# Optimization experiments

Hardware: AMD Instinct MI355X
Metric: run time of the kernel (lower is better)

The kernel has to match this reference:

```python
import jax, jax.numpy as jnp
import numpy as np

B, T, D_MODEL, HEAD = 4, 4096, 1024, 64

def setup_inputs() -> dict:
    key = jax.random.key(0)
    ks = jax.random.split(key, 7)
    s = 0.02  # typical init scale
    return {
        "x":  jax.random.normal(ks[0], (B, T, D_MODEL), dtype=jnp.float32),
        "Wq": jax.random.normal(ks[1], (D_MODEL, HEAD), dtype=jnp.float32) * s,
        "bq": jnp.zeros((HEAD,), dtype=jnp.float32),
        "Wk": jax.random.normal(ks[2], (D_MODEL, HEAD), dtype=jnp.float32) * s,
        "bk": jnp.zeros((HEAD,), dtype=jnp.float32),
        "Wv": jax.random.normal(ks[3], (D_MODEL, HEAD), dtype=jnp.float32) * s,
        "bv": jnp.zeros((HEAD,), dtype=jnp.float32),
    }

def reference(x, Wq, bq, Wk, bk, Wv, bv):
    Bz, Tz, C = x.shape
    q = x @ Wq + bq                      # (B,T,H)
    k = x @ Wk + bk                      # (B,T,H)
    v = x @ Wv + bv                      # (B,T,H)
    # NOTE: original scales by sqrt(C) = sqrt(d_model), not sqrt(head_size)
    att = jnp.einsum("bth,bsh->bts", q, k) / jnp.sqrt(jnp.float32(C))
    causal = jnp.tril(jnp.ones((Tz, Tz), dtype=bool))
    att = jnp.where(causal, att, -jnp.inf)
    att = jax.nn.softmax(att, axis=-1)
    return jnp.einsum("bts,bsh->bth", att, v)  # (B,T,H)
```

## Files before the change

### kernel.cpp

```cpp
#include <hip/hip_runtime.h>
#include <hip/hip_bf16.h>
#include <hip/hip_fp16.h>

#define T_SEQ 4096
#define DMODEL 1024
#define HEAD 64
#define NBATCH 4
#define NSEG 544
#define S2LOG 0.04508422f

typedef __attribute__((ext_vector_type(8))) short bf16x8;
typedef __attribute__((ext_vector_type(4))) float f32x4;

__device__ __forceinline__ unsigned short f2bf(float f) {
    unsigned int b = __float_as_uint(f);
    unsigned int r = b + 0x7FFFu + ((b >> 16) & 1u);
    return (unsigned short)(r >> 16);
}
__device__ __forceinline__ unsigned int pk_bf16(float a, float b) {
    __hip_bfloat162 h = __float22bfloat162_rn(make_float2(a, b));
    unsigned int u; __builtin_memcpy(&u, &h, 4); return u;
}
__device__ __forceinline__ void dma16(const void* g, void* s) {
    __builtin_amdgcn_global_load_lds(
        (const __attribute__((address_space(1))) unsigned int*)g,
        (__attribute__((address_space(3))) unsigned int*)s, 16, 0, 0);
}

__global__ __launch_bounds__(256) void prep_w(
    const float* __restrict__ Wq, const float* __restrict__ Wk,
    const float* __restrict__ Wv, unsigned short* __restrict__ Wtb)
{
    __shared__ unsigned short tl[64 * 72];
    const int bid = blockIdx.x;
    const int m   = bid >> 4;
    const int k0  = (bid & 15) * 64;
    const float* W = (m == 0) ? Wq : (m == 1) ? Wk : Wv;
    const int t  = threadIdx.x;
    const int kr = t >> 2, qtr = t & 3;
#pragma unroll
    for (int i = 0; i < 4; ++i) {
        float4 wv4 = *(const float4*)&W[(k0 + kr) * 64 + qtr * 16 + i * 4];
        tl[(qtr * 16 + i * 4 + 0) * 72 + kr] = f2bf(wv4.x);
        tl[(qtr * 16 + i * 4 + 1) * 72 + kr] = f2bf(wv4.y);
        tl[(qtr * 16 + i * 4 + 2) * 72 + kr] = f2bf(wv4.z);
        tl[(qtr * 16 + i * 4 + 3) * 72 + kr] = f2bf(wv4.w);
    }
    __syncthreads();
#pragma unroll
    for (int c = 0; c < 2; ++c) {
        const int lin = c * 256 + t;
        const int n = lin >> 3, k8 = lin & 7;
        *(uint4*)&Wtb[((long)(m * 64 + n)) * 1024 + k0 + k8 * 8] =
            *(const uint4*)&tl[n * 72 + k8 * 8];
    }
}

__global__ __launch_bounds__(256, 3) void qkv_mfma(
    const float* __restrict__ x, const unsigned short* __restrict__ Wtb,
    const float* __restrict__ bq, const float* __restrict__ bk,
    const float* __restrict__ bv,
    unsigned short* __restrict__ qo, unsigned short* __restrict__ ko,
    unsigned short* __restrict__ vt)
{
    __shared__ __align__(16) float xs[2][4096];
    const int t    = threadIdx.x;
    const int lane = t & 63;
    const int l15  = lane & 15, quad = lane >> 4;
    const int w    = __builtin_amdgcn_readfirstlane(t >> 6);
    const long row0 = (long)blockIdx.x * 32;

    float bias[3];
#pragma unroll
    for (int ntl = 0; ntl < 3; ++ntl) {
        const int c = w * 48 + ntl * 16 + l15;
        bias[ntl] = (c < 64) ? bq[c] : (c < 128) ? bk[c - 64] : bv[c - 128];
    }
    f32x4 acc[2][3];
#pragma unroll
    for (int mt = 0; mt < 2; ++mt)
#pragma unroll
        for (int ntl = 0; ntl < 3; ++ntl)
            acc[mt][ntl] = (f32x4){bias[ntl], bias[ntl], bias[ntl], bias[ntl]};

    auto dma_stage = [&](int sg, int buf) {
#pragma unroll
        for (int i = 0; i < 4; ++i) {
            const int jj  = w * 4 + i;
            const int row = jj * 2 + (lane >> 5);
            const int lgb = (lane & 31) ^ (row & 7);
            dma16(x + (row0 + row) * DMODEL + sg * 128 + lgb * 4,
                  &xs[buf][jj * 256]);
        }
    };
    dma_stage(0, 0);

    for (int sg = 0; sg < 8; ++sg) {
        __syncthreads();
        if (sg + 1 < 8) dma_stage(sg + 1, (sg + 1) & 1);
        bf16x8 wf[3][4];
#pragma unroll
        for (int ntl = 0; ntl < 3; ++ntl)
#pragma unroll
            for (int kq = 0; kq < 4; ++kq)
                wf[ntl][kq] = *(const bf16x8*)&Wtb[((long)(w * 48 + ntl * 16 + l15)) * 1024
                                                   + sg * 128 + kq * 32 + quad * 8];
#pragma unroll
        for (int mt = 0; mt < 2; ++mt)
#pragma unroll
            for (int kq = 0; kq < 4; ++kq) {
                const int row  = mt * 16 + l15;
                const int b0   = (kq * 8 + quad * 2)     ^ (row & 7);
                const int b1   = (kq * 8 + quad * 2 + 1) ^ (row & 7);
                float4 a0 = *(const float4*)&xs[sg & 1][row * 128 + b0 * 4];
                float4 a1 = *(const float4*)&xs[sg & 1][row * 128 + b1 * 4];
                unsigned int u[4];
                u[0] = pk_bf16(a0.x, a0.y); u[1] = pk_bf16(a0.z, a0.w);
                u[2] = pk_bf16(a1.x, a1.y); u[3] = pk_bf16(a1.z, a1.w);
                bf16x8 a; __builtin_memcpy(&a, u, 16);
#pragma unroll
                for (int ntl = 0; ntl < 3; ++ntl)
                    acc[mt][ntl] = __builtin_amdgcn_mfma_f32_16x16x32_bf16(a, wf[ntl][kq], acc[mt][ntl], 0, 0, 0);
            }
    }
#pragma unroll
    for (int mt = 0; mt < 2; ++mt)
#pragma unroll
        for (int ntl = 0; ntl < 3; ++ntl) {
            const int c = w * 48 + ntl * 16 + l15;
            const long tr0 = row0 + mt * 16 + quad * 4;
            if (c < 64) {
#pragma unroll
                for (int r = 0; r < 4; ++r)
                    qo[(tr0 + r) * HEAD + c] = f2bf(acc[mt][ntl][r] * S2LOG);
            } else if (c < 128) {
#pragma unroll
                for (int r = 0; r < 4; ++r)
                    ko[(tr0 + r) * HEAD + (c - 64)] = f2bf(acc[mt][ntl][r]);
            } else {
                const int b = (int)(tr0 >> 12), tloc = (int)(tr0 & 4095);
                uint2 pv;
                pv.x = pk_bf16(acc[mt][ntl][0], acc[mt][ntl][1]);
                pv.y = pk_bf16(acc[mt][ntl][2], acc[mt][ntl][3]);
                *(uint2*)&vt[((long)(b * HEAD + (c - 128))) * T_SEQ + tloc] = pv;
            }
        }
}

__global__ __launch_bounds__(256, 3) void flash_seg(
    const unsigned short* __restrict__ qg,
    const unsigned short* __restrict__ kg,
    const unsigned short* __restrict__ vtg,
    __half* __restrict__ opart, float* __restrict__ ml)
{
    __shared__ __align__(16) unsigned short kv_s[2][8192];
    __shared__ __align__(16) unsigned short p_s[4][16 * 72];
    const int t0   = threadIdx.x;
    const int lane = t0 & 63;
    const int l15  = lane & 15, quad = lane >> 4;
    const int wv   = __builtin_amdgcn_readfirstlane(t0 >> 6);

    const int bid = (int)blockIdx.x;
    const int sid = (NSEG - 1) - (bid >> 2);
    const int b   = bid & 3;

    int kk = 0, pref = 0;
#pragma unroll
    for (int i = 0; i < 15; ++i) {
        const int cnt = 4 * (kk + 1);
        if (sid >= pref + cnt) { pref += cnt; ++kk; }
    }
    const int S   = kk + 1;
    const int rem = sid - pref;
    const int t   = kk * 4 + rem / S;
    const int si  = rem % S;
    const int r0  = t * 64;
    const int rw  = r0 + wv * 16;
    const int nck = t + 1;
    const int c0  = (si * nck) / S, c1 = ((si + 1) * nck) / S;
    const long bbase = (long)b * T_SEQ;
    const int gidx = b * NSEG + sid;

    bf16x8 qf[2];
#pragma unroll
    for (int h = 0; h < 2; ++h)
        qf[h] = *(const bf16x8*)&qg[(bbase + rw + l15) * HEAD + h * 32 + quad * 8];

    f32x4 o[4];
#pragma unroll
    for (int dt = 0; dt < 4; ++dt) o[dt] = (f32x4){0.f, 0.f, 0.f, 0.f};
    float lrun = 0.f;
    unsigned short* ps = p_s[wv];

    auto dma_chunk = [&](int key0, int buf) {
#pragma unroll
        for (int i = 0; i < 2; ++i) {
            const int jj  = wv * 2 + i;
            const int kl  = jj * 8 + (lane >> 3);
            const int dlg = (lane & 7) ^ ((lane >> 3) & 7);
            dma16(kg + (bbase + key0 + kl) * HEAD + dlg * 8,
                  &kv_s[buf][jj * 512]);
        }
#pragma unroll
        for (int i = 0; i < 2; ++i) {
            const int jj  = wv * 2 + i;
            const int dim = jj * 8 + (lane >> 3);
            const int klg = (lane & 7) ^ ((lane >> 3) & 7);
            dma16(vtg + ((long)(b * HEAD + dim)) * T_SEQ + key0 + klg * 8,
                  &kv_s[buf][4096 + jj * 512]);
        }
    };
    dma_chunk(c0 * 64, 0);

    for (int c = c0; c < c1; ++c) {
        const int key0 = c * 64;
        const int cur  = (c - c0) & 1;
        __syncthreads();
        if (c + 1 < c1) dma_chunk((c + 1) * 64, cur ^ 1);

        f32x4 st[4];
#pragma unroll
        for (int mt = 0; mt < 4; ++mt) {
            const int key_l = mt * 16 + l15;
            bf16x8 k0 = *(const bf16x8*)&kv_s[cur][key_l * 64 + ((quad    ) ^ (l15 & 7)) * 8];
            bf16x8 k1 = *(const bf16x8*)&kv_s[cur][key_l * 64 + ((quad + 4) ^ (l15 & 7)) * 8];
            f32x4 z = (f32x4){0.f, 0.f, 0.f, 0.f};
            z = __builtin_amdgcn_mfma_f32_16x16x32_bf16(k0, qf[0], z, 0, 0, 0);
            st[mt] = __builtin_amdgcn_mfma_f32_16x16x32_bf16(k1, qf[1], st[mt] = z, 0, 0, 0);
        }
        bf16x8 vf[4][2];
#pragma unroll
        for (int dt = 0; dt < 4; ++dt) {
            const int dim = dt * 16 + l15;
            vf[dt][0] = *(const bf16x8*)&kv_s[cur][4096 + dim * 64 + ((quad    ) ^ (l15 & 7)) * 8];
            vf[dt][1] = *(const bf16x8*)&kv_s[cur][4096 + dim * 64 + ((quad + 4) ^ (l15 & 7)) * 8];
        }
        if (key0 + 63 > rw) {
            const int row = rw + l15;
#pragma unroll
            for (int mt = 0; mt < 4; ++mt)
#pragma unroll
                for (int r = 0; r < 4; ++r) {
                    const int key = key0 + mt * 16 + quad * 4 + r;
                    st[mt][r] = (key <= row) ? st[mt][r] : -30000.f;
                }
        }
        float psum = 0.f;
#pragma unroll
        for (int mt = 0; mt < 4; ++mt) {
            float e0 = exp2f(st[mt][0]), e1 = exp2f(st[mt][1]);
            float e2 = exp2f(st[mt][2]), e3 = exp2f(st[mt][3]);
            psum += (e0 + e1) + (e2 + e3);
            *(unsigned int*)&ps[l15 * 72 + mt * 16 + quad * 4]     = pk_bf16(e0, e1);
            *(unsigned int*)&ps[l15 * 72 + mt * 16 + quad * 4 + 2] = pk_bf16(e2, e3);
        }
        psum += __shfl_xor(psum, 16);
        psum += __shfl_xor(psum, 32);
        lrun += psum;
        __builtin_amdgcn_wave_barrier();
        bf16x8 pf[2];
#pragma unroll
        for (int g = 0; g < 2; ++g)
            pf[g] = *(const bf16x8*)&ps[l15 * 72 + g * 32 + quad * 8];
        __builtin_amdgcn_wave_barrier();
#pragma unroll
        for (int dt = 0; dt < 4; ++dt) {
            o[dt] = __builtin_amdgcn_mfma_f32_16x16x32_bf16(vf[dt][0], pf[0], o[dt], 0, 0, 0);
            o[dt] = __builtin_amdgcn_mfma_f32_16x16x32_bf16(vf[dt][1], pf[1], o[dt], 0, 0, 0);
        }
    }

    const float inv = (lrun > 0.f) ? 1.f / lrun : 0.f;
    __half* op = opart + (long)gidx * 4096;
#pragma unroll
    for (int dt = 0; dt < 4; ++dt) {
        __half2 h0 = __floats2half2_rn(o[dt][0] * inv, o[dt][1] * inv);
        __half2 h1 = __floats2half2_rn(o[dt][2] * inv, o[dt][3] * inv);
        uint2 u; __builtin_memcpy(&u.x, &h0, 4); __builtin_memcpy(&u.y, &h1, 4);
        *(uint2*)&op[(wv * 16 + l15) * HEAD + dt * 16 + quad * 4] = u;
    }
    if (quad == 0)
        ml[(long)gidx * 64 + wv * 16 + l15] = lrun;
}

__global__ __launch_bounds__(256) void merge_seg(
    const __half* __restrict__ opart, const float* __restrict__ ml,
    float* __restrict__ out)
{
    const int bid = blockIdx.x;
    const int t = bid & 63, b = bid >> 6;
    const int kk = t >> 2, S = kk + 1;
    const int base_sid = 2 * kk * (kk + 1) + (t & 3) * S;
    const int tid = threadIdx.x;
    const int row = tid >> 2, col0 = (tid & 3) * 16;

    float acc[16];
#pragma unroll
    for (int j = 0; j < 16; ++j) acc[j] = 0.f;
    float L = 0.f;
    for (int si = 0; si < S; ++si) {
        const long g = (long)(b * NSEG + base_sid + si);
        const float l = ml[g * 64 + row];
        L += l;
        const __half* op = opart + g * 4096 + row * 64 + col0;
#pragma unroll
        for (int h = 0; h < 2; ++h) {
            uint4 u = *(const uint4*)(op + h * 8);
            __half2 h01, h23, h45, h67;
            __builtin_memcpy(&h01, &u.x, 4); __builtin_memcpy(&h23, &u.y, 4);
            __builtin_memcpy(&h45, &u.z, 4); __builtin_memcpy(&h67, &u.w, 4);
            float2 f01 = __half22float2(h01), f23 = __half22float2(h23);
            float2 f45 = __half22float2(h45), f67 = __half22float2(h67);
            acc[h * 8 + 0] += l * f01.x; acc[h * 8 + 1] += l * f01.y;
            acc[h * 8 + 2] += l * f23.x; acc[h * 8 + 3] += l * f23.y;
            acc[h * 8 + 4] += l * f45.x; acc[h * 8 + 5] += l * f45.y;
            acc[h * 8 + 6] += l * f67.x; acc[h * 8 + 7] += l * f67.y;
        }
    }
    const float inv = 1.f / L;
    float* dst = out + ((long)(b * T_SEQ + t * 64 + row)) * HEAD + col0;
#pragma unroll
    for (int h = 0; h < 4; ++h) {
        float4 ov = {acc[h * 4] * inv, acc[h * 4 + 1] * inv,
                     acc[h * 4 + 2] * inv, acc[h * 4 + 3] * inv};
        *(float4*)(dst + h * 4) = ov;
    }
}

extern "C" void kernel_launch(void* const* d_in, const int* in_sizes, int n_in,
                              void* d_out, int out_size, void* d_ws, size_t ws_size,
                              hipStream_t stream) {
    const float* x  = (const float*)d_in[0];
    const float* Wq = (const float*)d_in[1];
    const float* bq = (const float*)d_in[2];
    const float* Wk = (const float*)d_in[3];
    const float* bk = (const float*)d_in[4];
    const float* Wv = (const float*)d_in[5];
    const float* bv = (const float*)d_in[6];
    float* outp = (float*)d_out;

    char* wsb = (char*)d_ws;
    unsigned short* wtb = (unsigned short*)(wsb);
    unsigned short* qw  = (unsigned short*)(wsb + 393216);
    unsigned short* kw  = (unsigned short*)(wsb + 2490368);
    unsigned short* vtw = (unsigned short*)(wsb + 4587520);
    __half* opart       = (__half*)(wsb + 6684672);
    float*  mlp         = (float*)(wsb + 24510464);

    prep_w<<<dim3(48), dim3(256), 0, stream>>>(Wq, Wk, Wv, wtb);
    qkv_mfma<<<dim3(512), dim3(256), 0, stream>>>(
        x, wtb, bq, bk, bv, qw, kw, vtw);
    flash_seg<<<dim3(NSEG * NBATCH), dim3(256), 0, stream>>>(qw, kw, vtw, opart, mlp);
    merge_seg<<<dim3(256), dim3(256), 0, stream>>>(opart, mlp, outp);
}
```

Baseline: 157.7 us.

## Stage x as bf16 in LDS via register prefetch; split merge blocks in half

```diff
diff --git a/kernel.cpp b/kernel.cpp
--- a/kernel.cpp
+++ b/kernel.cpp
@@ -63,7 +63,7 @@
     unsigned short* __restrict__ qo, unsigned short* __restrict__ ko,
     unsigned short* __restrict__ vt)
 {
-    __shared__ __align__(16) float xs[2][4096];
+    __shared__ __align__(16) unsigned short xs[2][4096];
     const int t    = threadIdx.x;
     const int lane = t & 63;
     const int l15  = lane & 15, quad = lane >> 4;
@@ -83,21 +83,31 @@
         for (int ntl = 0; ntl < 3; ++ntl)
             acc[mt][ntl] = (f32x4){bias[ntl], bias[ntl], bias[ntl], bias[ntl]};
 
-    auto dma_stage = [&](int sg, int buf) {
-#pragma unroll
-        for (int i = 0; i < 4; ++i) {
-            const int jj  = w * 4 + i;
-            const int row = jj * 2 + (lane >> 5);
-            const int lgb = (lane & 31) ^ (row & 7);
-            dma16(x + (row0 + row) * DMODEL + sg * 128 + lgb * 4,
-                  &xs[buf][jj * 256]);
+    float4 g[4];
+    auto load_stage = [&](int sg) {
+#pragma unroll
+        for (int s = 0; s < 4; ++s) {
+            const int id = s * 256 + t, row = id >> 5, off = id & 31;
+            g[s] = *(const float4*)&x[(row0 + row) * DMODEL + sg * 128 + off * 4];
         }
     };
-    dma_stage(0, 0);
+    auto write_stage = [&](int buf) {
+#pragma unroll
+        for (int s = 0; s < 4; ++s) {
+            const int id = s * 256 + t, row = id >> 5, off = id & 31;
+            uint2 u;
+            u.x = pk_bf16(g[s].x, g[s].y);
+            u.y = pk_bf16(g[s].z, g[s].w);
+            *(uint2*)&xs[buf][row * 128 + ((off >> 1) ^ (row & 7)) * 8 + (off & 1) * 4] = u;
+        }
+    };
+
+    load_stage(0);
+    write_stage(0);
 
     for (int sg = 0; sg < 8; ++sg) {
         __syncthreads();
-        if (sg + 1 < 8) dma_stage(sg + 1, (sg + 1) & 1);
+        if (sg + 1 < 8) load_stage(sg + 1);
         bf16x8 wf[3][4];
 #pragma unroll
         for (int ntl = 0; ntl < 3; ++ntl)
@@ -109,19 +119,14 @@
         for (int mt = 0; mt < 2; ++mt)
 #pragma unroll
             for (int kq = 0; kq < 4; ++kq) {
-                const int row  = mt * 16 + l15;
-                const int b0   = (kq * 8 + quad * 2)     ^ (row & 7);
-                const int b1   = (kq * 8 + quad * 2 + 1) ^ (row & 7);
-                float4 a0 = *(const float4*)&xs[sg & 1][row * 128 + b0 * 4];
-                float4 a1 = *(const float4*)&xs[sg & 1][row * 128 + b1 * 4];
-                unsigned int u[4];
-                u[0] = pk_bf16(a0.x, a0.y); u[1] = pk_bf16(a0.z, a0.w);
-                u[2] = pk_bf16(a1.x, a1.y); u[3] = pk_bf16(a1.z, a1.w);
-                bf16x8 a; __builtin_memcpy(&a, u, 16);
+                const int row = mt * 16 + l15;
+                bf16x8 a = *(const bf16x8*)&xs[sg & 1][row * 128
+                                                       + ((kq * 4 + quad) ^ (row & 7)) * 8];
 #pragma unroll
                 for (int ntl = 0; ntl < 3; ++ntl)
                     acc[mt][ntl] = __builtin_amdgcn_mfma_f32_16x16x32_bf16(a, wf[ntl][kq], acc[mt][ntl], 0, 0, 0);
             }
+        if (sg + 1 < 8) write_stage((sg + 1) & 1);
     }
 #pragma unroll
     for (int mt = 0; mt < 2; ++mt)
@@ -288,39 +293,36 @@
     float* __restrict__ out)
 {
     const int bid = blockIdx.x;
-    const int t = bid & 63, b = bid >> 6;
+    const int half = bid & 1, t = (bid >> 1) & 63, b = bid >> 7;
     const int kk = t >> 2, S = kk + 1;
     const int base_sid = 2 * kk * (kk + 1) + (t & 3) * S;
     const int tid = threadIdx.x;
-    const int row = tid >> 2, col0 = (tid & 3) * 16;
-
-    float acc[16];
-#pragma unroll
-    for (int j = 0; j < 16; ++j) acc[j] = 0.f;
+    const int row = half * 32 + (tid >> 3), col0 = (tid & 7) * 8;
+
+    float acc[8];
+#pragma unroll
+    for (int j = 0; j < 8; ++j) acc[j] = 0.f;
     float L = 0.f;
     for (int si = 0; si < S; ++si) {
         const long g = (long)(b * NSEG + base_sid + si);
         const float l = ml[g * 64 + row];
         L += l;
         const __half* op = opart + g * 4096 + row * 64 + col0;
-#pragma unroll
-        for (int h = 0; h < 2; ++h) {
-            uint4 u = *(const uint4*)(op + h * 8);
-            __half2 h01, h23, h45, h67;
-            __builtin_memcpy(&h01, &u.x, 4); __builtin_memcpy(&h23, &u.y, 4);
-            __builtin_memcpy(&h45, &u.z, 4); __builtin_memcpy(&h67, &u.w, 4);
-            float2 f01 = __half22float2(h01), f23 = __half22float2(h23);
-            float2 f45 = __half22float2(h45), f67 = __half22float2(h67);
-            acc[h * 8 + 0] += l * f01.x; acc[h * 8 + 1] += l * f01.y;
-            acc[h * 8 + 2] += l * f23.x; acc[h * 8 + 3] += l * f23.y;
-            acc[h * 8 + 4] += l * f45.x; acc[h * 8 + 5] += l * f45.y;
-            acc[h * 8 + 6] += l * f67.x; acc[h * 8 + 7] += l * f67.y;
-        }
+        uint4 u = *(const uint4*)op;
+        __half2 h01, h23, h45, h67;
+        __builtin_memcpy(&h01, &u.x, 4); __builtin_memcpy(&h23, &u.y, 4);
+        __builtin_memcpy(&h45, &u.z, 4); __builtin_memcpy(&h67, &u.w, 4);
+        float2 f01 = __half22float2(h01), f23 = __half22float2(h23);
+        float2 f45 = __half22float2(h45), f67 = __half22float2(h67);
+        acc[0] += l * f01.x; acc[1] += l * f01.y;
+        acc[2] += l * f23.x; acc[3] += l * f23.y;
+        acc[4] += l * f45.x; acc[5] += l * f45.y;
+        acc[6] += l * f67.x; acc[7] += l * f67.y;
     }
     const float inv = 1.f / L;
     float* dst = out + ((long)(b * T_SEQ + t * 64 + row)) * HEAD + col0;
 #pragma unroll
-    for (int h = 0; h < 4; ++h) {
+    for (int h = 0; h < 2; ++h) {
         float4 ov = {acc[h * 4] * inv, acc[h * 4 + 1] * inv,
                      acc[h * 4 + 2] * inv, acc[h * 4 + 3] * inv};
         *(float4*)(dst + h * 4) = ov;
@@ -351,5 +353,5 @@
     qkv_mfma<<<dim3(512), dim3(256), 0, stream>>>(
         x, wtb, bq, bk, bv, qw, kw, vtw);
     flash_seg<<<dim3(NSEG * NBATCH), dim3(256), 0, stream>>>(qw, kw, vtw, opart, mlp);
-    merge_seg<<<dim3(256), dim3(256), 0, stream>>>(opart, mlp, outp);
-}
+    merge_seg<<<dim3(512), dim3(256), 0, stream>>>(opart, mlp, outp);
+}
```

Result: no change. 157.6 us (-0.0%).
